# Kernel optimization log

Measured on AMD Instinct MI355X. Metric: run time of the kernel, lower is better.

## Reference

```python
import jax, jax.numpy as jnp
import numpy as np

# ---- fixed config (mirrors init_kwargs) ----
NUM_CLASSES = 4
A = 36          # num anchors per location
H, W = 48, 160  # feature map size
STRIDE = 16
N = H * W * A   # 276480 rois per image
B = 4
G = 32          # padded GT slots per image
FG_LO, BG_HI, IGN_LO, BEST_LO = 0.5, 0.5, 0.5, 0.35
BBOX_MEANS = jnp.zeros((4,), jnp.float32)
BBOX_STDS = jnp.array([0.1, 0.1, 0.2, 0.2], jnp.float32)
BBOX_2D_LAMBDA = 1.0
IOU_2D_LAMBDA = 1.0


def _xywh(boxes):
    w = boxes[..., 2] - boxes[..., 0] + 1.0
    h = boxes[..., 3] - boxes[..., 1] + 1.0
    cx = boxes[..., 0] + 0.5 * w
    cy = boxes[..., 1] + 0.5 * h
    return cx, cy, w, h


def iou_matrix(a, b):
    # a [M,4], b [K,4] -> IoU [M,K]
    x1 = jnp.maximum(a[:, None, 0], b[None, :, 0])
    y1 = jnp.maximum(a[:, None, 1], b[None, :, 1])
    x2 = jnp.minimum(a[:, None, 2], b[None, :, 2])
    y2 = jnp.minimum(a[:, None, 3], b[None, :, 3])
    inter = jnp.maximum(x2 - x1 + 1.0, 0.0) * jnp.maximum(y2 - y1 + 1.0, 0.0)
    area_a = (a[:, 2] - a[:, 0] + 1.0) * (a[:, 3] - a[:, 1] + 1.0)
    area_b = (b[:, 2] - b[:, 0] + 1.0) * (b[:, 3] - b[:, 1] + 1.0)
    return inter / jnp.maximum(area_a[:, None] + area_b[None, :] - inter, 1e-6)


def inter_over_a(a, b):
    # intersection / area(a): 'ign' overlap mode  [M,K]
    x1 = jnp.maximum(a[:, None, 0], b[None, :, 0])
    y1 = jnp.maximum(a[:, None, 1], b[None, :, 1])
    x2 = jnp.minimum(a[:, None, 2], b[None, :, 2])
    y2 = jnp.minimum(a[:, None, 3], b[None, :, 3])
    inter = jnp.maximum(x2 - x1 + 1.0, 0.0) * jnp.maximum(y2 - y1 + 1.0, 0.0)
    area_a = (a[:, 2] - a[:, 0] + 1.0) * (a[:, 3] - a[:, 1] + 1.0)
    return inter / jnp.maximum(area_a[:, None], 1e-6)


def iou_list(a, b):
    # elementwise IoU of matching boxes (mode='list')
    x1 = jnp.maximum(a[..., 0], b[..., 0])
    y1 = jnp.maximum(a[..., 1], b[..., 1])
    x2 = jnp.minimum(a[..., 2], b[..., 2])
    y2 = jnp.minimum(a[..., 3], b[..., 3])
    inter = jnp.maximum(x2 - x1 + 1.0, 0.0) * jnp.maximum(y2 - y1 + 1.0, 0.0)
    area_a = (a[..., 2] - a[..., 0] + 1.0) * (a[..., 3] - a[..., 1] + 1.0)
    area_b = (b[..., 2] - b[..., 0] + 1.0) * (b[..., 3] - b[..., 1] + 1.0)
    return inter / jnp.maximum(area_a + area_b - inter, 1e-6)


def bbox_transform(rois, gts):
    rcx, rcy, rw, rh = _xywh(rois)
    gcx, gcy, gw, gh = _xywh(gts)
    dx = (gcx - rcx) / rw
    dy = (gcy - rcy) / rh
    dw = jnp.log(jnp.maximum(gw, 1.0) / rw)
    dh = jnp.log(jnp.maximum(gh, 1.0) / rh)
    return jnp.stack([dx, dy, dw, dh], axis=-1)


def bbox_transform_inv(rois, deltas):
    # deltas are in normalized space; denormalize with means/stds as in source
    d = deltas * BBOX_STDS + BBOX_MEANS
    rcx, rcy, rw, rh = _xywh(rois)
    cx = rcx + d[..., 0] * rw
    cy = rcy + d[..., 1] * rh
    w = jnp.exp(d[..., 2]) * rw
    h = jnp.exp(d[..., 3]) * rh
    return jnp.stack([cx - 0.5 * w, cy - 0.5 * h,
                      cx + 0.5 * w - 1.0, cy + 0.5 * h - 1.0], axis=-1)


def setup_inputs() -> dict:
    key = jax.random.key(0)
    ks = jax.random.split(key, 10)
    cls = jax.random.normal(ks[0], (B, N, NUM_CLASSES), jnp.float32)
    prob = jax.nn.softmax(jax.random.normal(ks[1], (B, N, NUM_CLASSES), jnp.float32), axis=-1)
    bbox_x = 0.3 * jax.random.normal(ks[2], (B, N), jnp.float32)
    bbox_y = 0.3 * jax.random.normal(ks[3], (B, N), jnp.float32)
    bbox_w = 0.3 * jax.random.normal(ks[4], (B, N), jnp.float32)
    bbox_h = 0.3 * jax.random.normal(ks[5], (B, N), jnp.float32)
    # anchors: 12 scales x 3 aspect ratios = 36 (M3D-RPN style), then locate on grid
    scales = np.array([32.0 * (1.26 ** i) for i in range(12)])
    ratios = np.array([0.5, 1.0, 1.5])
    ws = (scales[:, None] * np.sqrt(ratios)[None, :]).reshape(-1)
    hs = (scales[:, None] / np.sqrt(ratios)[None, :]).reshape(-1)
    anchors = np.stack([-(ws - 1) / 2, -(hs - 1) / 2, (ws - 1) / 2, (hs - 1) / 2], axis=1)
    sx, sy = np.meshgrid(np.arange(W) * STRIDE, np.arange(H) * STRIDE)  # [H,W]
    shifts = np.stack([sx, sy, sx, sy], axis=-1).reshape(-1, 1, 4)      # [H*W,1,4]
    rois = jnp.asarray((shifts + anchors[None]).reshape(-1, 4), jnp.float32)  # [N,4]
    # padded GT boxes with validity/ignore masks
    cx = jax.random.uniform(ks[6], (B, G)) * W * STRIDE
    cy = jax.random.uniform(ks[7], (B, G)) * H * STRIDE
    gw = 20.0 + 280.0 * jax.random.uniform(ks[8], (B, G))
    gh = 20.0 + 280.0 * jax.random.uniform(ks[9], (B, G))
    gts_boxes = jnp.stack([cx - gw / 2, cy - gh / 2, cx + gw / 2, cy + gh / 2], -1).astype(jnp.float32)
    r = jax.random.randint(jax.random.fold_in(key, 1), (B, G), 0, 4)
    gts_val = (r < 2).astype(jnp.int32)
    gts_ign = (r == 2).astype(jnp.int32)
    gts_cls = jax.random.randint(jax.random.fold_in(key, 2), (B, G), 1, NUM_CLASSES).astype(jnp.int32)
    return {"cls": cls, "prob": prob, "bbox_x": bbox_x, "bbox_y": bbox_y,
            "bbox_w": bbox_w, "bbox_h": bbox_h, "rois": rois,
            "gts_boxes": gts_boxes, "gts_cls": gts_cls,
            "gts_val": gts_val, "gts_ign": gts_ign}


def reference(cls, prob, bbox_x, bbox_y, bbox_w, bbox_h, rois,
              gts_boxes, gts_cls, gts_val, gts_ign):
    def assign(gb, gc, gv, gi):
        # gb [G,4], gc/gv/gi [G]
        ol = iou_matrix(rois, gb)                       # [N,G]
        olv = jnp.where(gv[None, :] > 0, ol, -1.0)
        max_ol = olv.max(axis=1)                        # [N]
        tgt = olv.argmax(axis=1)                        # [N]
        oli = inter_over_a(rois, gb)                    # ignore-mode overlap
        max_ign = jnp.where(gi[None, :] > 0, oli, -1.0).max(axis=1)
        # best-anchor-per-GT assignment (compute_targets best_thresh path)
        best_ol = olv.max(axis=0)                       # [G]
        best_idx = olv.argmax(axis=0)                   # [G]
        take = (best_ol >= BEST_LO) & (gv > 0)
        scat = jnp.where(take, best_idx, N)             # padded scatter drop slot
        fg_best = jnp.zeros(N + 1, bool).at[scat].set(True)[:N]
        tgt_best = jnp.zeros(N + 1, jnp.int32).at[scat].set(jnp.arange(G, dtype=jnp.int32))[:N]
        fg = (max_ol >= FG_LO) | fg_best
        tgt = jnp.where(fg_best, tgt_best, tgt)
        ign = (~fg) & (max_ign >= IGN_LO)
        bg = (~fg) & (~ign)
        labels = jnp.where(fg, gc[tgt], 0).astype(jnp.int32)
        t = (bbox_transform(rois, gb[tgt]) - BBOX_MEANS) / BBOX_STDS  # [N,4]
        t = jnp.where(fg[:, None], t, 0.0)
        return labels, fg, bg, t

    labels, fg, bg, tnorm = jax.vmap(assign)(gts_boxes, gts_cls, gts_val, gts_ign)
    # classification cross-entropy over active (fg | bg) anchors
    logp = jax.nn.log_softmax(cls, axis=-1)                        # [B,N,C]
    ce = -jnp.take_along_axis(logp, labels[..., None], axis=-1)[..., 0]
    active = (fg | bg).astype(ce.dtype)
    cls_loss = (ce * active).sum() / jnp.maximum(active.sum(), 1.0)
    d = jnp.stack([bbox_x, bbox_y, bbox_w, bbox_h], axis=-1)       # [B,N,4]
    diff = jnp.abs(d - tnorm)
    sl1 = jnp.where(diff < 1.0, 0.5 * diff * diff, diff - 0.5).sum(-1)
    fgf = fg.astype(sl1.dtype)
    nfg = jnp.maximum(fgf.sum(), 1.0)
    bbox_loss = BBOX_2D_LAMBDA * (sl1 * fgf).sum() / nfg
    # 2D IoU loss between decoded predictions and decoded targets (fg only)
    cpred = bbox_transform_inv(rois, d)
    ctar = bbox_transform_inv(rois, tnorm)
    iou2d = iou_list(cpred, ctar)                                  # [B,N]
    safe_iou = jnp.clip(jnp.where(fg, iou2d, 1.0), 1e-6, 1.0)
    iou_loss = IOU_2D_LAMBDA * (-jnp.log(safe_iou) * fgf).sum() / nfg
    return cls_loss + bbox_loss + iou_loss
```

## Files before the change

### kernel.cpp

```cpp
#include <hip/hip_runtime.h>

#define N_ANCH 276480
#define BATCH  4
#define NGT    32
#define NBLK   (N_ANCH / 256)

#define XMARG 249.0f
#define YMARG 288.0f

__device__ __forceinline__ float waveReduce(float v) {
    for (int o = 32; o; o >>= 1) v += __shfl_down(v, o);
    return v;
}

__device__ __forceinline__ void wave_bbox(int n, float& wx1, float& wy1,
                                          float& wx2, float& wy2) {
    const int nw0 = n & ~63;
    const int loc0 = nw0 / 36;
    const int loc1 = (nw0 + 63) / 36;
    const int y0 = loc0 / 160, x0 = loc0 - y0 * 160;
    const int y1 = loc1 / 160, x1 = loc1 - y1 * 160;
    float xmin, xmax;
    if (y0 != y1) { xmin = 0.f; xmax = 159.f * 16.f; }
    else          { xmin = (float)(x0 * 16); xmax = (float)(x1 * 16); }
    wx1 = xmin - XMARG; wx2 = xmax + XMARG;
    wy1 = (float)(y0 * 16) - YMARG; wy2 = (float)(y1 * 16) + YMARG;
}

__global__ __launch_bounds__(256) void rpn_best(
    const float4* __restrict__ rois,
    const float4* __restrict__ gtb,
    const int* __restrict__ gval_g,
    unsigned long long* __restrict__ keys)
{
    __shared__ float gx1[NGT], gy1[NGT], gx2[NGT], gy2[NGT], garea[NGT];
    __shared__ int gval[NGT];
    const int tid = threadIdx.x;
    const int b = blockIdx.y;
    if (tid < NGT) {
        float4 g = gtb[b * NGT + tid];
        gx1[tid] = g.x; gy1[tid] = g.y; gx2[tid] = g.z; gy2[tid] = g.w;
        garea[tid] = (g.z - g.x + 1.f) * (g.w - g.y + 1.f);
        gval[tid] = gval_g[b * NGT + tid];
    }
    __syncthreads();
    const int n = blockIdx.x * 256 + tid;
    float4 r = rois[n];
    const float ra = (r.z - r.x + 1.f) * (r.w - r.y + 1.f);
    float wx1, wy1, wx2, wy2;
    wave_bbox(n, wx1, wy1, wx2, wy2);
    const int lane = tid & 63;
    bool inc = false;
    if (lane < NGT) {
        bool ov = (fminf(wx2, gx2[lane]) - fmaxf(wx1, gx1[lane]) + 1.f > 0.f)
               && (fminf(wy2, gy2[lane]) - fmaxf(wy1, gy1[lane]) + 1.f > 0.f);
        inc = ov && (gval[lane] > 0);
    }
    unsigned m = (unsigned)__ballot(inc);
    while (m) {
        const int g = __ffs(m) - 1; m &= m - 1;
        float ix1 = fmaxf(r.x, gx1[g]), iy1 = fmaxf(r.y, gy1[g]);
        float ix2 = fminf(r.z, gx2[g]), iy2 = fminf(r.w, gy2[g]);
        float inter = fmaxf(ix2 - ix1 + 1.f, 0.f) * fmaxf(iy2 - iy1 + 1.f, 0.f);
        float S = ra + garea[g];
        if (inter >= 0.25f * S) {
            float iou = inter / fmaxf(S - inter, 1e-6f);
            if (iou >= 0.35f) {
                unsigned long long key =
                    ((unsigned long long)__float_as_uint(iou) << 32) |
                    (unsigned long long)(0xFFFFFFFFu - (unsigned)n);
                atomicMax(&keys[b * NGT + g], key);
            }
        }
    }
}

__global__ __launch_bounds__(256) void rpn_main(
    const float4* __restrict__ cls,
    const float* __restrict__ bx, const float* __restrict__ by,
    const float* __restrict__ bw, const float* __restrict__ bh,
    const float4* __restrict__ rois,
    const float4* __restrict__ gtb,
    const int* __restrict__ gcls_g, const int* __restrict__ gval_g,
    const int* __restrict__ gign_g,
    const unsigned long long* __restrict__ keys,
    float* __restrict__ partials)
{
    __shared__ float gx1[NGT], gy1[NGT], gx2[NGT], gy2[NGT], garea[NGT];
    __shared__ int gcls[NGT], gval[NGT], gign[NGT];
    __shared__ unsigned bidx[NGT];
    __shared__ float wred[4 * 5];
    const int tid = threadIdx.x;
    const int b = blockIdx.y;
    if (tid < NGT) {
        float4 g = gtb[b * NGT + tid];
        gx1[tid] = g.x; gy1[tid] = g.y; gx2[tid] = g.z; gy2[tid] = g.w;
        garea[tid] = (g.z - g.x + 1.f) * (g.w - g.y + 1.f);
        gcls[tid] = gcls_g[b * NGT + tid];
        gval[tid] = gval_g[b * NGT + tid];
        gign[tid] = gign_g[b * NGT + tid];
        unsigned long long k = keys[b * NGT + tid];
        bidx[tid] = k ? (0xFFFFFFFFu - (unsigned)(k & 0xFFFFFFFFull)) : 0xFFFFFFFFu;
    }
    __syncthreads();
    const int n = blockIdx.x * 256 + tid;
    float4 r = rois[n];
    const float rw = r.z - r.x + 1.f, rh = r.w - r.y + 1.f;
    const float ra = rw * rh;
    float wx1, wy1, wx2, wy2;
    wave_bbox(n, wx1, wy1, wx2, wy2);
    const int lane = tid & 63;
    bool incV = false, incI = false;
    if (lane < NGT) {
        bool ov = (fminf(wx2, gx2[lane]) - fmaxf(wx1, gx1[lane]) + 1.f > 0.f)
               && (fminf(wy2, gy2[lane]) - fmaxf(wy1, gy1[lane]) + 1.f > 0.f);
        incV = ov && (gval[lane] > 0);
        incI = ov && (gign[lane] > 0);
    }
    const unsigned maskV = (unsigned)__ballot(incV);
    const unsigned maskI = (unsigned)__ballot(incI);
    unsigned m = maskV | maskI;

    float imax = -1.f, Smax = 1.f, ignInter = 0.f;
    int tgt = 0, tgtb = 0;
    bool fgbest = false;
    while (m) {
        const int g = __ffs(m) - 1; m &= m - 1;
        float ix1 = fmaxf(r.x, gx1[g]), iy1 = fmaxf(r.y, gy1[g]);
        float ix2 = fminf(r.z, gx2[g]), iy2 = fminf(r.w, gy2[g]);
        float inter = fmaxf(ix2 - ix1 + 1.f, 0.f) * fmaxf(iy2 - iy1 + 1.f, 0.f);
        if ((maskV >> g) & 1u) {
            float S = ra + garea[g];
            if (inter * Smax > imax * S) { imax = inter; Smax = S; tgt = g; }
            if (bidx[g] == (unsigned)n) { fgbest = true; tgtb = g; }
        }
        if ((maskI >> g) & 1u)
            ignInter = fmaxf(ignInter, inter);
    }
    const float olmax = imax / fmaxf(Smax - imax, 1e-6f);
    const bool fg = (olmax >= 0.5f) || fgbest;
    if (fgbest) tgt = tgtb;
    const float ignIoU = ignInter / fmaxf(ra, 1e-6f);
    const bool active = fg || (ignIoU < 0.5f);
    const int label = fg ? gcls[tgt] : 0;

    float4 c4 = cls[(size_t)b * N_ANCH + n];
    float c[4] = {c4.x, c4.y, c4.z, c4.w};
    float mx = fmaxf(fmaxf(c[0], c[1]), fmaxf(c[2], c[3]));
    float lse = mx + __logf(__expf(c[0] - mx) + __expf(c[1] - mx) +
                            __expf(c[2] - mx) + __expf(c[3] - mx));
    float ce = lse - c[label];
    float ceS = active ? ce : 0.f;
    float sl1S = 0.f, iouS = 0.f;

    if (fg) {
        const float rcx = r.x + 0.5f * rw, rcy = r.y + 0.5f * rh;
        const float gw_ = gx2[tgt] - gx1[tgt] + 1.f;
        const float gh_ = gy2[tgt] - gy1[tgt] + 1.f;
        const float gcx = gx1[tgt] + 0.5f * gw_;
        const float gcy = gy1[tgt] + 0.5f * gh_;
        const float t0 = ((gcx - rcx) / rw) / 0.1f;
        const float t1 = ((gcy - rcy) / rh) / 0.1f;
        const float t2 = __logf(fmaxf(gw_, 1.f) / rw) / 0.2f;
        const float t3 = __logf(fmaxf(gh_, 1.f) / rh) / 0.2f;
        const size_t i = (size_t)b * N_ANCH + n;
        const float d0 = bx[i], d1 = by[i], d2 = bw[i], d3 = bh[i];
        float a0 = fabsf(d0 - t0), a1 = fabsf(d1 - t1);
        float a2 = fabsf(d2 - t2), a3 = fabsf(d3 - t3);
        sl1S = (a0 < 1.f ? 0.5f * a0 * a0 : a0 - 0.5f)
             + (a1 < 1.f ? 0.5f * a1 * a1 : a1 - 0.5f)
             + (a2 < 1.f ? 0.5f * a2 * a2 : a2 - 0.5f)
             + (a3 < 1.f ? 0.5f * a3 * a3 : a3 - 0.5f);
        float pcx = rcx + d0 * 0.1f * rw, pcy = rcy + d1 * 0.1f * rh;
        float pw = __expf(d2 * 0.2f) * rw, ph = __expf(d3 * 0.2f) * rh;
        float px1 = pcx - 0.5f * pw, py1 = pcy - 0.5f * ph;
        float px2 = pcx + 0.5f * pw - 1.f, py2 = pcy + 0.5f * ph - 1.f;
        float tcx = rcx + t0 * 0.1f * rw, tcy = rcy + t1 * 0.1f * rh;
        float tw = __expf(t2 * 0.2f) * rw, th = __expf(t3 * 0.2f) * rh;
        float tx1 = tcx - 0.5f * tw, ty1 = tcy - 0.5f * th;
        float tx2 = tcx + 0.5f * tw - 1.f, ty2 = tcy + 0.5f * th - 1.f;
        float ix1 = fmaxf(px1, tx1), iy1 = fmaxf(py1, ty1);
        float ix2 = fminf(px2, tx2), iy2 = fminf(py2, ty2);
        float inter = fmaxf(ix2 - ix1 + 1.f, 0.f) * fmaxf(iy2 - iy1 + 1.f, 0.f);
        float pa = (px2 - px1 + 1.f) * (py2 - py1 + 1.f);
        float ta = (tx2 - tx1 + 1.f) * (ty2 - ty1 + 1.f);
        float iou2 = inter / fmaxf(pa + ta - inter, 1e-6f);
        float safe = fminf(fmaxf(iou2, 1e-6f), 1.f);
        iouS = -__logf(safe);
    }

    const float actW = (float)__popcll(__ballot(active));
    const float fgW  = (float)__popcll(__ballot(fg));
    const int wave = tid >> 6;
    {
        float v0 = waveReduce(ceS);
        float v2 = waveReduce(sl1S);
        float v4 = waveReduce(iouS);
        if (lane == 0) {
            wred[wave * 5 + 0] = v0; wred[wave * 5 + 1] = actW;
            wred[wave * 5 + 2] = v2; wred[wave * 5 + 3] = fgW;
            wred[wave * 5 + 4] = v4;
        }
    }
    __syncthreads();
    if (tid == 0) {
        float* p = &partials[(size_t)(b * NBLK + blockIdx.x) * 5];
        #pragma unroll
        for (int k = 0; k < 5; ++k)
            p[k] = wred[k] + wred[5 + k] + wred[10 + k] + wred[15 + k];
    }
}

__global__ __launch_bounds__(256) void rpn_final(
    const float* __restrict__ partials, float* __restrict__ out)
{
    __shared__ float wred[4 * 5];
    const int tid = threadIdx.x;
    float s[5] = {0.f, 0.f, 0.f, 0.f, 0.f};
    for (int i = tid; i < BATCH * NBLK; i += 256) {
        const float* p = &partials[(size_t)i * 5];
        #pragma unroll
        for (int k = 0; k < 5; ++k) s[k] += p[k];
    }
    const int wave = tid >> 6, lane = tid & 63;
    #pragma unroll
    for (int k = 0; k < 5; ++k) {
        float v = waveReduce(s[k]);
        if (lane == 0) wred[wave * 5 + k] = v;
    }
    __syncthreads();
    if (tid == 0) {
        float t[5];
        #pragma unroll
        for (int k = 0; k < 5; ++k)
            t[k] = wred[k] + wred[5 + k] + wred[10 + k] + wred[15 + k];
        float cls_loss = t[0] / fmaxf(t[1], 1.f);
        float nfg = fmaxf(t[3], 1.f);
        out[0] = cls_loss + t[2] / nfg + t[4] / nfg;
    }
}

extern "C" void kernel_launch(void* const* d_in, const int* in_sizes, int n_in,
                              void* d_out, int out_size, void* d_ws, size_t ws_size,
                              hipStream_t stream) {
    const float4* cls  = (const float4*)d_in[0];
    const float*  bx   = (const float*)d_in[2];
    const float*  by   = (const float*)d_in[3];
    const float*  bw   = (const float*)d_in[4];
    const float*  bh   = (const float*)d_in[5];
    const float4* rois = (const float4*)d_in[6];
    const float4* gtb  = (const float4*)d_in[7];
    const int* gcls = (const int*)d_in[8];
    const int* gval = (const int*)d_in[9];
    const int* gign = (const int*)d_in[10];

    unsigned long long* keys = (unsigned long long*)d_ws;
    float* partials = (float*)((char*)d_ws + 1024);
    float* out = (float*)d_out;

    hipMemsetAsync(d_ws, 0, 1024, stream);
    dim3 grid(NBLK, BATCH);
    rpn_best<<<grid, dim3(256), 0, stream>>>(rois, gtb, gval, keys);
    rpn_main<<<grid, dim3(256), 0, stream>>>(cls, bx, by, bw, bh, rois, gtb,
                                             gcls, gval, gign, keys, partials);
    rpn_final<<<dim3(1), dim3(256), 0, stream>>>(partials, out);
}
```

Before: 128.3 us.

## Fuse best-anchor pass into main pass and apply correction in final kernel

Removes the separate rpn_best pass over all anchors. The main kernel now computes each anchor's normal fg/bg assignment while also doing the atomicMax best-anchor search. The final single-block kernel then recomputes the few best-anchor winners (up to one per GT) and adds delta corrections for their forced-fg label, regression and IoU terms. This drops one full kernel launch and one read of the rois, trading it for serial per-GT recomputation in the final kernel.

Result: slower. 144.0 us (+12.3%).

```diff
diff --git a/kernel.cpp b/kernel.cpp
--- a/kernel.cpp
+++ b/kernel.cpp
@@ -27,55 +27,51 @@
     wy1 = (float)(y0 * 16) - YMARG; wy2 = (float)(y1 * 16) + YMARG;
 }
 
-__global__ __launch_bounds__(256) void rpn_best(
-    const float4* __restrict__ rois,
-    const float4* __restrict__ gtb,
-    const int* __restrict__ gval_g,
-    unsigned long long* __restrict__ keys)
+__device__ __forceinline__ float lse4(float4 c4) {
+    float mx = fmaxf(fmaxf(c4.x, c4.y), fmaxf(c4.z, c4.w));
+    return mx + __logf(__expf(c4.x - mx) + __expf(c4.y - mx) +
+                       __expf(c4.z - mx) + __expf(c4.w - mx));
+}
+
+__device__ __forceinline__ void fg_terms(
+    float rx, float ry, float rz, float rwc, float rw, float rh,
+    float Gx1, float Gy1, float Gx2, float Gy2,
+    float d0, float d1, float d2, float d3,
+    float& sl1S, float& iouS)
 {
-    __shared__ float gx1[NGT], gy1[NGT], gx2[NGT], gy2[NGT], garea[NGT];
-    __shared__ int gval[NGT];
-    const int tid = threadIdx.x;
-    const int b = blockIdx.y;
-    if (tid < NGT) {
-        float4 g = gtb[b * NGT + tid];
-        gx1[tid] = g.x; gy1[tid] = g.y; gx2[tid] = g.z; gy2[tid] = g.w;
-        garea[tid] = (g.z - g.x + 1.f) * (g.w - g.y + 1.f);
-        gval[tid] = gval_g[b * NGT + tid];
-    }
-    __syncthreads();
-    const int n = blockIdx.x * 256 + tid;
-    float4 r = rois[n];
-    const float ra = (r.z - r.x + 1.f) * (r.w - r.y + 1.f);
-    float wx1, wy1, wx2, wy2;
-    wave_bbox(n, wx1, wy1, wx2, wy2);
-    const int lane = tid & 63;
-    bool inc = false;
-    if (lane < NGT) {
-        bool ov = (fminf(wx2, gx2[lane]) - fmaxf(wx1, gx1[lane]) + 1.f > 0.f)
-               && (fminf(wy2, gy2[lane]) - fmaxf(wy1, gy1[lane]) + 1.f > 0.f);
-        inc = ov && (gval[lane] > 0);
-    }
-    unsigned m = (unsigned)__ballot(inc);
-    while (m) {
-        const int g = __ffs(m) - 1; m &= m - 1;
-        float ix1 = fmaxf(r.x, gx1[g]), iy1 = fmaxf(r.y, gy1[g]);
-        float ix2 = fminf(r.z, gx2[g]), iy2 = fminf(r.w, gy2[g]);
-        float inter = fmaxf(ix2 - ix1 + 1.f, 0.f) * fmaxf(iy2 - iy1 + 1.f, 0.f);
-        float S = ra + garea[g];
-        if (inter >= 0.25f * S) {
-            float iou = inter / fmaxf(S - inter, 1e-6f);
-            if (iou >= 0.35f) {
-                unsigned long long key =
-                    ((unsigned long long)__float_as_uint(iou) << 32) |
-                    (unsigned long long)(0xFFFFFFFFu - (unsigned)n);
-                atomicMax(&keys[b * NGT + g], key);
-            }
-        }
-    }
-}
-
-__global__ __launch_bounds__(256) void rpn_main(
+    const float rcx = rx + 0.5f * rw, rcy = ry + 0.5f * rh;
+    const float gw_ = Gx2 - Gx1 + 1.f, gh_ = Gy2 - Gy1 + 1.f;
+    const float gcx = Gx1 + 0.5f * gw_, gcy = Gy1 + 0.5f * gh_;
+    const float t0 = ((gcx - rcx) / rw) / 0.1f;
+    const float t1 = ((gcy - rcy) / rh) / 0.1f;
+    const float t2 = __logf(fmaxf(gw_, 1.f) / rw) / 0.2f;
+    const float t3 = __logf(fmaxf(gh_, 1.f) / rh) / 0.2f;
+    float a0 = fabsf(d0 - t0), a1 = fabsf(d1 - t1);
+    float a2 = fabsf(d2 - t2), a3 = fabsf(d3 - t3);
+    sl1S = (a0 < 1.f ? 0.5f * a0 * a0 : a0 - 0.5f)
+         + (a1 < 1.f ? 0.5f * a1 * a1 : a1 - 0.5f)
+         + (a2 < 1.f ? 0.5f * a2 * a2 : a2 - 0.5f)
+         + (a3 < 1.f ? 0.5f * a3 * a3 : a3 - 0.5f);
+    float pcx = rcx + d0 * 0.1f * rw, pcy = rcy + d1 * 0.1f * rh;
+    float pw = __expf(d2 * 0.2f) * rw, ph = __expf(d3 * 0.2f) * rh;
+    float px1 = pcx - 0.5f * pw, py1 = pcy - 0.5f * ph;
+    float px2 = pcx + 0.5f * pw - 1.f, py2 = pcy + 0.5f * ph - 1.f;
+    float tcx = rcx + t0 * 0.1f * rw, tcy = rcy + t1 * 0.1f * rh;
+    float tw = __expf(t2 * 0.2f) * rw, th = __expf(t3 * 0.2f) * rh;
+    float tx1 = tcx - 0.5f * tw, ty1 = tcy - 0.5f * th;
+    float tx2 = tcx + 0.5f * tw - 1.f, ty2 = tcy + 0.5f * th - 1.f;
+    float ix1 = fmaxf(px1, tx1), iy1 = fmaxf(py1, ty1);
+    float ix2 = fminf(px2, tx2), iy2 = fminf(py2, ty2);
+    float inter = fmaxf(ix2 - ix1 + 1.f, 0.f) * fmaxf(iy2 - iy1 + 1.f, 0.f);
+    float pa = (px2 - px1 + 1.f) * (py2 - py1 + 1.f);
+    float ta = (tx2 - tx1 + 1.f) * (ty2 - ty1 + 1.f);
+    float iou2 = inter / fmaxf(pa + ta - inter, 1e-6f);
+    float safe = fminf(fmaxf(iou2, 1e-6f), 1.f);
+    iouS = -__logf(safe);
+    (void)rz; (void)rwc;
+}
+
+__global__ __launch_bounds__(256) void rpn_fused(
     const float4* __restrict__ cls,
     const float* __restrict__ bx, const float* __restrict__ by,
     const float* __restrict__ bw, const float* __restrict__ bh,
@@ -83,12 +79,11 @@
     const float4* __restrict__ gtb,
     const int* __restrict__ gcls_g, const int* __restrict__ gval_g,
     const int* __restrict__ gign_g,
-    const unsigned long long* __restrict__ keys,
+    unsigned long long* __restrict__ keys,
     float* __restrict__ partials)
 {
     __shared__ float gx1[NGT], gy1[NGT], gx2[NGT], gy2[NGT], garea[NGT];
     __shared__ int gcls[NGT], gval[NGT], gign[NGT];
-    __shared__ unsigned bidx[NGT];
     __shared__ float wred[4 * 5];
     const int tid = threadIdx.x;
     const int b = blockIdx.y;
@@ -99,8 +94,6 @@
         gcls[tid] = gcls_g[b * NGT + tid];
         gval[tid] = gval_g[b * NGT + tid];
         gign[tid] = gign_g[b * NGT + tid];
-        unsigned long long k = keys[b * NGT + tid];
-        bidx[tid] = k ? (0xFFFFFFFFu - (unsigned)(k & 0xFFFFFFFFull)) : 0xFFFFFFFFu;
     }
     __syncthreads();
     const int n = blockIdx.x * 256 + tid;
@@ -122,8 +115,7 @@
     unsigned m = maskV | maskI;
 
     float imax = -1.f, Smax = 1.f, ignInter = 0.f;
-    int tgt = 0, tgtb = 0;
-    bool fgbest = false;
+    int tgt = 0;
     while (m) {
         const int g = __ffs(m) - 1; m &= m - 1;
         float ix1 = fmaxf(r.x, gx1[g]), iy1 = fmaxf(r.y, gy1[g]);
@@ -132,61 +124,35 @@
         if ((maskV >> g) & 1u) {
             float S = ra + garea[g];
             if (inter * Smax > imax * S) { imax = inter; Smax = S; tgt = g; }
-            if (bidx[g] == (unsigned)n) { fgbest = true; tgtb = g; }
+            if (inter >= 0.25f * S) {
+                float iou = inter / fmaxf(S - inter, 1e-6f);
+                if (iou >= 0.35f) {
+                    unsigned long long key =
+                        ((unsigned long long)__float_as_uint(iou) << 32) |
+                        (unsigned long long)(0xFFFFFFFFu - (unsigned)n);
+                    atomicMax(&keys[b * NGT + g], key);
+                }
+            }
         }
         if ((maskI >> g) & 1u)
             ignInter = fmaxf(ignInter, inter);
     }
     const float olmax = imax / fmaxf(Smax - imax, 1e-6f);
-    const bool fg = (olmax >= 0.5f) || fgbest;
-    if (fgbest) tgt = tgtb;
+    const bool fg = (olmax >= 0.5f);
     const float ignIoU = ignInter / fmaxf(ra, 1e-6f);
     const bool active = fg || (ignIoU < 0.5f);
     const int label = fg ? gcls[tgt] : 0;
 
     float4 c4 = cls[(size_t)b * N_ANCH + n];
-    float c[4] = {c4.x, c4.y, c4.z, c4.w};
-    float mx = fmaxf(fmaxf(c[0], c[1]), fmaxf(c[2], c[3]));
-    float lse = mx + __logf(__expf(c[0] - mx) + __expf(c[1] - mx) +
-                            __expf(c[2] - mx) + __expf(c[3] - mx));
-    float ce = lse - c[label];
+    const float* c = (const float*)&c4;
+    float ce = lse4(c4) - c[label];
     float ceS = active ? ce : 0.f;
     float sl1S = 0.f, iouS = 0.f;
-
     if (fg) {
-        const float rcx = r.x + 0.5f * rw, rcy = r.y + 0.5f * rh;
-        const float gw_ = gx2[tgt] - gx1[tgt] + 1.f;
-        const float gh_ = gy2[tgt] - gy1[tgt] + 1.f;
-        const float gcx = gx1[tgt] + 0.5f * gw_;
-        const float gcy = gy1[tgt] + 0.5f * gh_;
-        const float t0 = ((gcx - rcx) / rw) / 0.1f;
-        const float t1 = ((gcy - rcy) / rh) / 0.1f;
-        const float t2 = __logf(fmaxf(gw_, 1.f) / rw) / 0.2f;
-        const float t3 = __logf(fmaxf(gh_, 1.f) / rh) / 0.2f;
         const size_t i = (size_t)b * N_ANCH + n;
-        const float d0 = bx[i], d1 = by[i], d2 = bw[i], d3 = bh[i];
-        float a0 = fabsf(d0 - t0), a1 = fabsf(d1 - t1);
-        float a2 = fabsf(d2 - t2), a3 = fabsf(d3 - t3);
-        sl1S = (a0 < 1.f ? 0.5f * a0 * a0 : a0 - 0.5f)
-             + (a1 < 1.f ? 0.5f * a1 * a1 : a1 - 0.5f)
-             + (a2 < 1.f ? 0.5f * a2 * a2 : a2 - 0.5f)
-             + (a3 < 1.f ? 0.5f * a3 * a3 : a3 - 0.5f);
-        float pcx = rcx + d0 * 0.1f * rw, pcy = rcy + d1 * 0.1f * rh;
-        float pw = __expf(d2 * 0.2f) * rw, ph = __expf(d3 * 0.2f) * rh;
-        float px1 = pcx - 0.5f * pw, py1 = pcy - 0.5f * ph;
-        float px2 = pcx + 0.5f * pw - 1.f, py2 = pcy + 0.5f * ph - 1.f;
-        float tcx = rcx + t0 * 0.1f * rw, tcy = rcy + t1 * 0.1f * rh;
-        float tw = __expf(t2 * 0.2f) * rw, th = __expf(t3 * 0.2f) * rh;
-        float tx1 = tcx - 0.5f * tw, ty1 = tcy - 0.5f * th;
-        float tx2 = tcx + 0.5f * tw - 1.f, ty2 = tcy + 0.5f * th - 1.f;
-        float ix1 = fmaxf(px1, tx1), iy1 = fmaxf(py1, ty1);
-        float ix2 = fminf(px2, tx2), iy2 = fminf(py2, ty2);
-        float inter = fmaxf(ix2 - ix1 + 1.f, 0.f) * fmaxf(iy2 - iy1 + 1.f, 0.f);
-        float pa = (px2 - px1 + 1.f) * (py2 - py1 + 1.f);
-        float ta = (tx2 - tx1 + 1.f) * (ty2 - ty1 + 1.f);
-        float iou2 = inter / fmaxf(pa + ta - inter, 1e-6f);
-        float safe = fminf(fmaxf(iou2, 1e-6f), 1.f);
-        iouS = -__logf(safe);
+        fg_terms(r.x, r.y, r.z, r.w, rw, rh,
+                 gx1[tgt], gy1[tgt], gx2[tgt], gy2[tgt],
+                 bx[i], by[i], bw[i], bh[i], sl1S, iouS);
     }
 
     const float actW = (float)__popcll(__ballot(active));
@@ -211,14 +177,105 @@
     }
 }
 
-__global__ __launch_bounds__(256) void rpn_final(
-    const float* __restrict__ partials, float* __restrict__ out)
+__global__ __launch_bounds__(256) void rpn_final_fix(
+    const float4* __restrict__ cls,
+    const float* __restrict__ bx, const float* __restrict__ by,
+    const float* __restrict__ bw, const float* __restrict__ bh,
+    const float4* __restrict__ rois,
+    const float4* __restrict__ gtb,
+    const int* __restrict__ gcls_g, const int* __restrict__ gval_g,
+    const int* __restrict__ gign_g,
+    const unsigned long long* __restrict__ keys,
+    const float* __restrict__ partials,
+    float* __restrict__ out)
 {
+    __shared__ float sgx1[BATCH*NGT], sgy1[BATCH*NGT], sgx2[BATCH*NGT],
+                     sgy2[BATCH*NGT], sgar[BATCH*NGT];
+    __shared__ int sgc[BATCH*NGT], sgv[BATCH*NGT], sgi[BATCH*NGT];
+    __shared__ unsigned candN[BATCH*NGT];
     __shared__ float wred[4 * 5];
     const int tid = threadIdx.x;
-    float s[5] = {0.f, 0.f, 0.f, 0.f, 0.f};
-    for (int i = tid; i < BATCH * NBLK; i += 256) {
-        const float* p = &partials[(size_t)i * 5];
+    unsigned myN = 0xFFFFFFFFu;
+    if (tid < BATCH * NGT) {
+        float4 G = gtb[tid];
+        sgx1[tid] = G.x; sgy1[tid] = G.y; sgx2[tid] = G.z; sgy2[tid] = G.w;
+        sgar[tid] = (G.z - G.x + 1.f) * (G.w - G.y + 1.f);
+        sgc[tid] = gcls_g[tid]; sgv[tid] = gval_g[tid]; sgi[tid] = gign_g[tid];
+        unsigned long long k = keys[tid];
+        if (k) {
+            float iou = __uint_as_float((unsigned)(k >> 32));
+            unsigned nn = 0xFFFFFFFFu - (unsigned)(k & 0xFFFFFFFFull);
+            if (iou >= 0.35f && nn < N_ANCH) myN = nn;
+        }
+        candN[tid] = myN;
+    }
+    __syncthreads();
+
+    float d0s = 0.f, d1s = 0.f, d2s = 0.f, d3s = 0.f, d4s = 0.f;
+    if (tid < BATCH * NGT && myN != 0xFFFFFFFFu) {
+        const int b = tid >> 5, g = tid & 31, base = b << 5;
+        bool winner = true;
+        for (int g2 = g + 1; g2 < NGT; ++g2)
+            if (candN[base + g2] == myN) { winner = false; break; }
+        if (winner) {
+            const int n = (int)myN;
+            float4 r = rois[n];
+            const float rw = r.z - r.x + 1.f, rh = r.w - r.y + 1.f;
+            const float ra = rw * rh;
+            float wx1, wy1, wx2, wy2;
+            wave_bbox(n, wx1, wy1, wx2, wy2);
+            float imax = -1.f, Smax = 1.f, ignInter = 0.f;
+            int tgt0 = 0;
+            for (int g2 = 0; g2 < NGT; ++g2) {
+                const int j = base + g2;
+                bool ov = (fminf(wx2, sgx2[j]) - fmaxf(wx1, sgx1[j]) + 1.f > 0.f)
+                       && (fminf(wy2, sgy2[j]) - fmaxf(wy1, sgy1[j]) + 1.f > 0.f);
+                bool v = ov && (sgv[j] > 0), iv = ov && (sgi[j] > 0);
+                if (!v && !iv) continue;
+                float ix1 = fmaxf(r.x, sgx1[j]), iy1 = fmaxf(r.y, sgy1[j]);
+                float ix2 = fminf(r.z, sgx2[j]), iy2 = fminf(r.w, sgy2[j]);
+                float inter = fmaxf(ix2 - ix1 + 1.f, 0.f) * fmaxf(iy2 - iy1 + 1.f, 0.f);
+                if (v) {
+                    float S = ra + sgar[j];
+                    if (inter * Smax > imax * S) { imax = inter; Smax = S; tgt0 = g2; }
+                }
+                if (iv) ignInter = fmaxf(ignInter, inter);
+            }
+            const float olmax = imax / fmaxf(Smax - imax, 1e-6f);
+            const bool fg0 = (olmax >= 0.5f);
+            const float ignIoU = ignInter / fmaxf(ra, 1e-6f);
+            const bool act0 = fg0 || (ignIoU < 0.5f);
+            float4 c4 = cls[(size_t)b * N_ANCH + n];
+            const float* c = (const float*)&c4;
+            const float lse = lse4(c4);
+            const int label0 = fg0 ? sgc[base + tgt0] : 0;
+            const float ce0 = act0 ? (lse - c[label0]) : 0.f;
+            const size_t i = (size_t)b * N_ANCH + n;
+            const float dd0 = bx[i], dd1 = by[i], dd2 = bw[i], dd3 = bh[i];
+            float sl1_0 = 0.f, iou_0 = 0.f;
+            if (fg0) {
+                const int j0 = base + tgt0;
+                fg_terms(r.x, r.y, r.z, r.w, rw, rh,
+                         sgx1[j0], sgy1[j0], sgx2[j0], sgy2[j0],
+                         dd0, dd1, dd2, dd3, sl1_0, iou_0);
+            }
+            const int j1 = base + g;
+            const float ce1 = lse - c[sgc[j1]];
+            float sl1_1, iou_1;
+            fg_terms(r.x, r.y, r.z, r.w, rw, rh,
+                     sgx1[j1], sgy1[j1], sgx2[j1], sgy2[j1],
+                     dd0, dd1, dd2, dd3, sl1_1, iou_1);
+            d0s = ce1 - ce0;
+            d1s = act0 ? 0.f : 1.f;
+            d2s = sl1_1 - sl1_0;
+            d3s = fg0 ? 0.f : 1.f;
+            d4s = iou_1 - iou_0;
+        }
+    }
+
+    float s[5] = {d0s, d1s, d2s, d3s, d4s};
+    for (int i2 = tid; i2 < BATCH * NBLK; i2 += 256) {
+        const float* p = &partials[(size_t)i2 * 5];
         #pragma unroll
         for (int k = 0; k < 5; ++k) s[k] += p[k];
     }
@@ -260,8 +317,9 @@
 
     hipMemsetAsync(d_ws, 0, 1024, stream);
     dim3 grid(NBLK, BATCH);
-    rpn_best<<<grid, dim3(256), 0, stream>>>(rois, gtb, gval, keys);
-    rpn_main<<<grid, dim3(256), 0, stream>>>(cls, bx, by, bw, bh, rois, gtb,
-                                             gcls, gval, gign, keys, partials);
-    rpn_final<<<dim3(1), dim3(256), 0, stream>>>(partials, out);
-}
+    rpn_fused<<<grid, dim3(256), 0, stream>>>(cls, bx, by, bw, bh, rois, gtb,
+                                              gcls, gval, gign, keys, partials);
+    rpn_final_fix<<<dim3(1), dim3(256), 0, stream>>>(cls, bx, by, bw, bh, rois,
+                                                     gtb, gcls, gval, gign,
+                                                     keys, partials, out);
+}
```
